# Kernel optimization log

Hardware: AMD Instinct MI355X
Metric: run time of the kernel (lower is better)

## Reference

```python
import jax, jax.numpy as jnp
import numpy as np
from jax import lax

FACTOR = 2
BLUR_K = [1.0, 3.0, 3.0, 1.0]

def _make_kernel(k, factor):
    k = jnp.asarray(k, dtype=jnp.float32)
    k = k[None, :] * k[:, None]          # outer product -> [4,4]
    k = k / jnp.sum(k)
    return k * (factor ** 2)

def setup_inputs() -> dict:
    key = jax.random.key(0)
    x = jax.random.normal(key, (32, 512, 512, 1), dtype=jnp.float32)  # NHWC, C must be 1
    kernel = _make_kernel(BLUR_K, FACTOR)                              # [4,4]
    return {"x": x, "kernel": kernel}

def reference(x, kernel):
    # nearest-neighbor upsample by FACTOR (matches tf.image.resize nearest for integer factor)
    up = jnp.repeat(jnpp if False else jnp.repeat(x, FACTOR, axis=1), FACTOR, axis=2)
    w = kernel.reshape(1, -1, 1, 1)  # [fh=1, fw=16, in=1, out=1] (HWIO)
    out = lax.conv_general_dilated(
        up, w,
        window_strides=(1, 1),
        padding='SAME',
        dimension_numbers=('NHWC', 'HWIO', 'NHWC'),
    )
    return out
```

## Files before the change

kernel.cpp:

```cpp
#include <hip/hip_runtime.h>


#define W_IN   512
#define H_IN   512
#define NB     32
#define W_OUT  1024
#define NPAIR  (NB * H_IN / 2)

typedef float f32x4 __attribute__((ext_vector_type(4)));

__global__ __launch_bounds__(256) void upsample_blur_kernel(
    const float* __restrict__ x,
    const float* __restrict__ kern,
    float* __restrict__ out)
{
    const int t    = threadIdx.x;
    const int rsel = t >> 7;
    const int s    = t & 127;

    const int p      = blockIdx.x;
    const int rowIn  = 2 * p + rsel;

    const float* xr = x + (size_t)rowIn * W_IN;
    const f32x4 zero = {0.f, 0.f, 0.f, 0.f};
    const f32x4 cA = (s == 0)   ? zero : *reinterpret_cast<const f32x4*>(xr + 4 * s - 4);
    const f32x4 cB =                     *reinterpret_cast<const f32x4*>(xr + 4 * s);
    const f32x4 cC = (s == 127) ? zero : *reinterpret_cast<const f32x4*>(xr + 4 * s + 4);

    float V[12];
    V[0] = cA.x; V[1]  = cA.y; V[2]  = cA.z; V[3]  = cA.w;
    V[4] = cB.x; V[5]  = cB.y; V[6]  = cB.z; V[7]  = cB.w;
    V[8] = cC.x; V[9]  = cC.y; V[10] = cC.z; V[11] = cC.w;

    float kf[16];
#pragma unroll
    for (int i = 0; i < 16; ++i) kf[i] = kern[i];

    float we[9], wo[8];
    we[0] = kf[0];
#pragma unroll
    for (int i = 0; i < 7; ++i) we[i + 1] = kf[2 * i + 1] + kf[2 * i + 2];
    we[8] = kf[15];
#pragma unroll
    for (int i = 0; i < 8; ++i) wo[i] = kf[2 * i] + kf[2 * i + 1];

    float o[8];
#pragma unroll
    for (int c = 0; c < 8; c += 2) {
        float accE = 0.f, accO = 0.f;
        const int se = c / 2;
        const int so = c / 2 + 1;
#pragma unroll
        for (int j = 0; j < 9; ++j) accE += we[j] * V[j + se];
#pragma unroll
        for (int j = 0; j < 8; ++j) accO += wo[j] * V[j + so];
        o[c]     = accE;
        o[c + 1] = accO;
    }

    f32x4 lo; lo.x = o[0]; lo.y = o[1]; lo.z = o[2]; lo.w = o[3];
    f32x4 hi; hi.x = o[4]; hi.y = o[5]; hi.z = o[6]; hi.w = o[7];

    const size_t ob = ((size_t)(4 * p + 2 * rsel)) * W_OUT + 8 * s;
    *reinterpret_cast<f32x4*>(out + ob)             = lo;
    *reinterpret_cast<f32x4*>(out + ob + 4)         = hi;
    *reinterpret_cast<f32x4*>(out + ob + W_OUT)     = lo;
    *reinterpret_cast<f32x4*>(out + ob + W_OUT + 4) = hi;
}

extern "C" void kernel_launch(void* const* d_in, const int* in_sizes, int n_in,
                              void* d_out, int out_size, void* d_ws, size_t ws_size,
                              hipStream_t stream) {
    const float* x    = (const float*)d_in[0];
    const float* kern = (const float*)d_in[1];
    float* out        = (float*)d_out;

    upsample_blur_kernel<<<NPAIR, 256, 0, stream>>>(x, kern, out);
}
```

Baseline: 158.2 us.

## Stage each input row in shared memory and compute four outputs per thread

Each block now handles one input row instead of a pair of rows. The row is loaded once into LDS with zero padding, and each thread reads a 10-element window from it to produce four outputs. This removes the redundant overlapping global loads and their halo branches, at the cost of a __syncthreads barrier, LDS traffic, and twice as many smaller blocks that each write 4 floats per thread per output row.

```diff
diff --git a/kernel.cpp b/kernel.cpp
--- a/kernel.cpp
+++ b/kernel.cpp
@@ -1,36 +1,30 @@
 #include <hip/hip_runtime.h>
 
 
-#define W_IN   512
-#define H_IN   512
-#define NB     32
-#define W_OUT  1024
-#define NPAIR  (NB * H_IN / 2)
-
-typedef float f32x4 __attribute__((ext_vector_type(4)));
+#define W_IN  512
+#define H_IN  512
+#define NB    32
+#define W_OUT 1024
 
 __global__ __launch_bounds__(256) void upsample_blur_kernel(
     const float* __restrict__ x,
     const float* __restrict__ kern,
     float* __restrict__ out)
 {
-    const int t    = threadIdx.x;
-    const int rsel = t >> 7;
-    const int s    = t & 127;
+    __shared__ float row[520];
 
-    const int p      = blockIdx.x;
-    const int rowIn  = 2 * p + rsel;
+    const int rowIdx = blockIdx.x;
+    const int n = rowIdx >> 9;
+    const int r = rowIdx & 511;
+    const int t = threadIdx.x;
 
-    const float* xr = x + (size_t)rowIn * W_IN;
-    const f32x4 zero = {0.f, 0.f, 0.f, 0.f};
-    const f32x4 cA = (s == 0)   ? zero : *reinterpret_cast<const f32x4*>(xr + 4 * s - 4);
-    const f32x4 cB =                     *reinterpret_cast<const f32x4*>(xr + 4 * s);
-    const f32x4 cC = (s == 127) ? zero : *reinterpret_cast<const f32x4*>(xr + 4 * s + 4);
+    if (t < 8) {
+        const int idx = (t < 4) ? t : (512 + t);
+        row[idx] = 0.0f;
+    }
 
-    float V[12];
-    V[0] = cA.x; V[1]  = cA.y; V[2]  = cA.z; V[3]  = cA.w;
-    V[4] = cB.x; V[5]  = cB.y; V[6]  = cB.z; V[7]  = cB.w;
-    V[8] = cC.x; V[9]  = cC.y; V[10] = cC.z; V[11] = cC.w;
+    const float* xrow = x + (size_t)(n * H_IN + r) * W_IN;
+    reinterpret_cast<float2*>(row + 4)[t] = reinterpret_cast<const float2*>(xrow)[t];
 
     float kf[16];
 #pragma unroll
@@ -44,28 +38,28 @@
 #pragma unroll
     for (int i = 0; i < 8; ++i) wo[i] = kf[2 * i] + kf[2 * i + 1];
 
-    float o[8];
+    __syncthreads();
+
+    float v[10];
 #pragma unroll
-    for (int c = 0; c < 8; c += 2) {
-        float accE = 0.f, accO = 0.f;
-        const int se = c / 2;
-        const int so = c / 2 + 1;
+    for (int i = 0; i < 10; ++i) v[i] = row[2 * t + i];
+
+    float o0 = 0.f, o1 = 0.f, o2 = 0.f, o3 = 0.f;
 #pragma unroll
-        for (int j = 0; j < 9; ++j) accE += we[j] * V[j + se];
+    for (int j = 0; j < 9; ++j) o0 += we[j] * v[j];
 #pragma unroll
-        for (int j = 0; j < 8; ++j) accO += wo[j] * V[j + so];
-        o[c]     = accE;
-        o[c + 1] = accO;
-    }
+    for (int j = 0; j < 8; ++j) o1 += wo[j] * v[j + 1];
+#pragma unroll
+    for (int j = 0; j < 9; ++j) o2 += we[j] * v[j + 1];
+#pragma unroll
+    for (int j = 0; j < 8; ++j) o3 += wo[j] * v[j + 2];
 
-    f32x4 lo; lo.x = o[0]; lo.y = o[1]; lo.z = o[2]; lo.w = o[3];
-    f32x4 hi; hi.x = o[4]; hi.y = o[5]; hi.z = o[6]; hi.w = o[7];
-
-    const size_t ob = ((size_t)(4 * p + 2 * rsel)) * W_OUT + 8 * s;
-    *reinterpret_cast<f32x4*>(out + ob)             = lo;
-    *reinterpret_cast<f32x4*>(out + ob + 4)         = hi;
-    *reinterpret_cast<f32x4*>(out + ob + W_OUT)     = lo;
-    *reinterpret_cast<f32x4*>(out + ob + W_OUT + 4) = hi;
+    const float4 o = make_float4(o0, o1, o2, o3);
+    const size_t outRowBase = ((size_t)n * W_OUT + 2 * r) * (size_t)W_OUT;
+    float4* out4a = reinterpret_cast<float4*>(out + outRowBase);
+    float4* out4b = reinterpret_cast<float4*>(out + outRowBase + W_OUT);
+    out4a[t] = o;
+    out4b[t] = o;
 }
 
 extern "C" void kernel_launch(void* const* d_in, const int* in_sizes, int n_in,
@@ -75,5 +69,6 @@
     const float* kern = (const float*)d_in[1];
     float* out        = (float*)d_out;
 
-    upsample_blur_kernel<<<NPAIR, 256, 0, stream>>>(x, kern, out);
+    const int numRows = NB * H_IN;
+    upsample_blur_kernel<<<numRows, 256, 0, stream>>>(x, kern, out);
 }
```

New measurement: 155.1 us. 1.02x faster.
